# Kernel optimization log

Measured on AMD Instinct MI355X. Metric: run time of the kernel, lower is better.

Reference implementation:

```python
import jax, jax.numpy as jnp
import numpy as np

D_MODEL = 2048
N_Q_HEADS = 32
N_KV_HEADS = 8
HEAD_DIM = D_MODEL // N_Q_HEADS  # 64
KV_DIM = HEAD_DIM * N_KV_HEADS   # 512
B, S = 2, 2048


def setup_inputs() -> dict:
    key = jax.random.key(0)
    ks = jax.random.split(key, 11)
    sc_d = 1.0 / np.sqrt(D_MODEL)
    return {
        "query": jax.random.normal(ks[0], (B, S, D_MODEL), jnp.float32),
        "key":   jax.random.normal(ks[1], (B, S, D_MODEL), jnp.float32),
        "value": jax.random.normal(ks[2], (B, S, D_MODEL), jnp.float32),
        "Wq": jax.random.normal(ks[3], (D_MODEL, D_MODEL), jnp.float32) * sc_d,
        "bq": jnp.zeros((D_MODEL,), jnp.float32),
        "Wk": jax.random.normal(ks[4], (D_MODEL, KV_DIM), jnp.float32) * sc_d,
        "bk": jnp.zeros((KV_DIM,), jnp.float32),
        "Wv": jax.random.normal(ks[5], (D_MODEL, KV_DIM), jnp.float32) * sc_d,
        "bv": jnp.zeros((KV_DIM,), jnp.float32),
        "Wo": jax.random.normal(ks[6], (D_MODEL, D_MODEL), jnp.float32) * sc_d,
        "bo": jnp.zeros((D_MODEL,), jnp.float32),
    }


def reference(query, key, value, Wq, bq, Wk, bk, Wv, bv, Wo, bo):
    b, s, _ = query.shape
    g = N_Q_HEADS // N_KV_HEADS  # num groups
    # projections
    Q = query @ Wq + bq                      # [b, s, d_model]
    K = key @ Wk + bk                        # [b, s, kv_dim]
    V = value @ Wv + bv                      # [b, s, kv_dim]
    # split heads. Torch code splits Q into groups of num_kv_heads heads,
    # and each group broadcasts per-head against the Hkv KV heads, i.e.
    # query head (grp*Hkv + j) attends against kv head j.
    Q = Q.reshape(b, s, g, N_KV_HEADS, HEAD_DIM)  # [b, s, g, hkv, d]
    K = K.reshape(b, s, N_KV_HEADS, HEAD_DIM)     # [b, s, hkv, d]
    V = V.reshape(b, s, N_KV_HEADS, HEAD_DIM)
    scale = 1.0 / jnp.sqrt(jnp.float32(HEAD_DIM))
    scores = jnp.einsum('bsghd,bthd->bghst', Q, K) * scale  # [b,g,hkv,s,s]
    attn = jax.nn.softmax(scores, axis=-1)
    out = jnp.einsum('bghst,bthd->bsghd', attn, V)          # [b,s,g,hkv,d]
    # concat over groups then heads == original head order (g major, hkv minor)
    out = out.reshape(b, s, D_MODEL)
    return out @ Wo + bo
```

## Files before the change

kernel.cpp:

```cpp
#include <hip/hip_runtime.h>
#include <cstdint>

typedef _Float16 half4 __attribute__((ext_vector_type(4)));
typedef _Float16 half8 __attribute__((ext_vector_type(8)));
typedef _Float16 half16 __attribute__((ext_vector_type(16)));
typedef float f32x4 __attribute__((ext_vector_type(4)));
typedef float f32x16 __attribute__((ext_vector_type(16)));

#define L2E 1.44269504088896340736f

__device__ __forceinline__ void gl16(const void* g, void* l) {
  __builtin_amdgcn_global_load_lds(
      (const __attribute__((address_space(1))) void*)g,
      (__attribute__((address_space(3))) void*)l, 16, 0, 0);
}

__device__ __forceinline__ uint32_t pk2(float a, float b) {
  return __builtin_bit_cast(uint32_t, __builtin_amdgcn_cvt_pkrtz(a, b));
}

__device__ __forceinline__ void plswap(uint32_t& x, uint32_t& y) {
  auto r = __builtin_amdgcn_permlane32_swap((int)x, (int)y, false, false);
  x = (uint32_t)r[0];
  y = (uint32_t)r[1];
}

__device__ __forceinline__ f32x16 zero16() {
  f32x16 z;
  #pragma unroll
  for (int r = 0; r < 16; ++r) z[r] = 0.0f;
  return z;
}

__global__ __launch_bounds__(256) void cvt_f32_f16_3(
    const float* __restrict__ s0, const float* __restrict__ s1, const float* __restrict__ s2,
    _Float16* __restrict__ d0, _Float16* __restrict__ d1, _Float16* __restrict__ d2)
{
  const float* src = (blockIdx.z == 0) ? s0 : (blockIdx.z == 1 ? s1 : s2);
  _Float16* dst    = (blockIdx.z == 0) ? d0 : (blockIdx.z == 1 ? d1 : d2);
  size_t i = ((size_t)blockIdx.x * 256 + threadIdx.x) * 8;
  float4 a = *(const float4*)(src + i);
  float4 b = *(const float4*)(src + i + 4);
  half8 o;
  o[0] = (_Float16)a.x; o[1] = (_Float16)a.y; o[2] = (_Float16)a.z; o[3] = (_Float16)a.w;
  o[4] = (_Float16)b.x; o[5] = (_Float16)b.y; o[6] = (_Float16)b.z; o[7] = (_Float16)b.w;
  *(half8*)(dst + i) = o;
}

__global__ __launch_bounds__(256) void transpose_w_all(
    const float* __restrict__ Wq, const float* __restrict__ Wk,
    const float* __restrict__ Wv, const float* __restrict__ Wo,
    _Float16* __restrict__ WqkvT, _Float16* __restrict__ WoT)
{
  int id = blockIdx.x;
  const float* src;
  _Float16* dst;
  int N, tx, ty;
  if (id < 4096)      { src = Wq; dst = WqkvT;                        N = 2048; tx = id & 63; ty = id >> 6; }
  else if (id < 5120) { id -= 4096; src = Wk; dst = WqkvT + (size_t)2048 * 2048; N = 512; tx = id & 15; ty = id >> 4; }
  else if (id < 6144) { id -= 5120; src = Wv; dst = WqkvT + (size_t)2560 * 2048; N = 512; tx = id & 15; ty = id >> 4; }
  else                { id -= 6144; src = Wo; dst = WoT;              N = 2048; tx = id & 63; ty = id >> 6; }
  const int n0 = tx * 32, k0 = ty * 32;
  __shared__ float t[32][33];
  #pragma unroll
  for (int i = 0; i < 4; ++i)
    t[threadIdx.y + i * 8][threadIdx.x] =
        src[(size_t)(k0 + threadIdx.y + i * 8) * N + n0 + threadIdx.x];
  __syncthreads();
  #pragma unroll
  for (int i = 0; i < 4; ++i)
    dst[(size_t)(n0 + threadIdx.y + i * 8) * 2048 + k0 + threadIdx.x] =
        (_Float16)t[threadIdx.x][threadIdx.y + i * 8];
}

__global__ __launch_bounds__(256) void transpose_v(
    const _Float16* __restrict__ QKV, _Float16* __restrict__ VT)
{
  const int bh = blockIdx.z;
  const int bb = bh >> 3, h = bh & 7;
  const int t0 = blockIdx.x * 32, d0 = blockIdx.y * 32;
  __shared__ _Float16 t[32][33];
  const _Float16* src = QKV + (size_t)(bb * 2048) * 3072 + 2560 + h * 64;
  #pragma unroll
  for (int i = 0; i < 4; ++i)
    t[threadIdx.y + i * 8][threadIdx.x] =
        src[(size_t)(t0 + threadIdx.y + i * 8) * 3072 + d0 + threadIdx.x];
  __syncthreads();
  _Float16* dst = VT + ((size_t)(bb * 8 + h) * 64) * 2048;
  #pragma unroll
  for (int i = 0; i < 4; ++i)
    dst[(size_t)(d0 + threadIdx.y + i * 8) * 2048 + t0 + threadIdx.x] =
        t[threadIdx.x][threadIdx.y + i * 8];
}

template<int MODE>
__global__ __launch_bounds__(512, 2) void gemm256(
    const _Float16* __restrict__ Aq, const _Float16* __restrict__ Ak, const _Float16* __restrict__ Av,
    const _Float16* __restrict__ Bt,
    const float* __restrict__ bias0, const float* __restrict__ bias1, const float* __restrict__ bias2,
    _Float16* __restrict__ Ch, float* __restrict__ Cf)
{
  constexpr int K = 2048;
  constexpr int N = (MODE == 0) ? 3072 : 2048;
  constexpr int NB = N / 256;
  constexpr int G = 16 * NB;

  const int wg = blockIdx.x;
  const int work = (wg & 7) * (G / 8) + (wg >> 3);
  const int m0 = (work / NB) * 256;
  const int n0 = (work % NB) * 256;

  const _Float16* A = Aq;
  if constexpr (MODE == 0) { if (n0 >= 2560) A = Av; else if (n0 >= 2048) A = Ak; }

  const int tid = threadIdx.x;
  const int lane = tid & 63;
  const int w = tid >> 6;
  const int wr = w >> 2;
  const int wc = w & 3;
  const int lo = lane & 15, hi = lane >> 4;

  __shared__ __align__(1024) char smem[98304];

  f32x4 acc[8][4];
  #pragma unroll
  for (int mt = 0; mt < 8; ++mt)
    #pragma unroll
    for (int nt = 0; nt < 4; ++nt)
      acc[mt][nt] = (f32x4){0.f, 0.f, 0.f, 0.f};

  const int srow = lane >> 2;
  const int sslot = lane & 3;
  const _Float16* pA = A  + (size_t)(m0 + w * 32 + srow) * K + sslot * 8;
  const _Float16* pB = Bt + (size_t)(n0 + w * 32 + srow) * K + sslot * 8;
  const size_t rstep = (size_t)16 * K;
  const int dst = w * 2048;

  {
    char* b0 = smem;
    char* b1 = smem + 32768;
    gl16(pA,            b0 + dst);          gl16(pA + rstep,            b0 + dst + 1024);
    gl16(pB,            b0 + 16384 + dst);  gl16(pB + rstep,            b0 + 16384 + dst + 1024);
    gl16(pA + 32,       b1 + dst);          gl16(pA + 32 + rstep,       b1 + dst + 1024);
    gl16(pB + 32,       b1 + 16384 + dst);  gl16(pB + 32 + rstep,       b1 + 16384 + dst + 1024);
  }
  pA += 64; pB += 64;
  asm volatile("s_waitcnt vmcnt(4)" ::: "memory");
  __builtin_amdgcn_s_barrier();

  const int abase = (wr * 128 + lo) * 64 + hi * 16;
  const int bbase = 16384 + (wc * 64 + lo) * 64 + hi * 16;

  int c = 0;
  for (int t = 0; t < 64; ++t) {
    int c1 = c + 1; if (c1 == 3) c1 = 0;
    int c2 = c1 + 1; if (c2 == 3) c2 = 0;
    if (t < 62) {
      char* bp = smem + (c2 << 15);
      gl16(pA,         bp + dst);          gl16(pA + rstep,         bp + dst + 1024);
      gl16(pB,         bp + 16384 + dst);  gl16(pB + rstep,         bp + 16384 + dst + 1024);
      pA += 32; pB += 32;
    }
    const char* bc = smem + (c << 15);
    half8 af[8], bf[4];
    #pragma unroll
    for (int mt = 0; mt < 8; ++mt) af[mt] = *(const half8*)(bc + abase + mt * 1024);
    #pragma unroll
    for (int nt = 0; nt < 4; ++nt) bf[nt] = *(const half8*)(bc + bbase + nt * 1024);
    __builtin_amdgcn_s_setprio(1);
    #pragma unroll
    for (int mt = 0; mt < 8; ++mt)
      #pragma unroll
      for (int nt = 0; nt < 4; ++nt)
        acc[mt][nt] = __builtin_amdgcn_mfma_f32_16x16x32_f16(af[mt], bf[nt], acc[mt][nt], 0, 0, 0);
    __builtin_amdgcn_s_setprio(0);
    if (t < 62)       asm volatile("s_waitcnt vmcnt(4)" ::: "memory");
    else if (t == 62) asm volatile("s_waitcnt vmcnt(0)" ::: "memory");
    if (t < 63) __builtin_amdgcn_s_barrier();
    c = c1;
  }

  float* T = (float*)smem;
  const int tr = tid >> 4;
  const int sc = tid & 15;
  #pragma unroll
  for (int mp = 0; mp < 8; ++mp) {
    __syncthreads();
    #pragma unroll
    for (int nt = 0; nt < 4; ++nt)
      #pragma unroll
      for (int r = 0; r < 4; ++r)
        T[(wr * 16 + 4 * hi + r) * 256 + wc * 64 + nt * 16 + lo] = acc[mp][nt][r];
    __syncthreads();
    const int grow = m0 + (tr >> 4) * 128 + mp * 16 + (tr & 15);
    const int gcol = n0 + sc * 16;
    const float* Trow = T + tr * 256 + sc * 16;
    float4 v[4];
    #pragma unroll
    for (int q = 0; q < 4; ++q) v[q] = ((const float4*)Trow)[q];
    const float* bp = bias0;
    int cb = gcol;
    if constexpr (MODE == 0) {
      if (gcol >= 2560) { bp = bias2; cb = gcol - 2560; }
      else if (gcol >= 2048) { bp = bias1; cb = gcol - 2048; }
    }
    float4 bvv[4];
    #pragma unroll
    for (int q = 0; q < 4; ++q) bvv[q] = ((const float4*)(bp + cb))[q];
    if constexpr (MODE == 0) {
      half16 o;
      #pragma unroll
      for (int q = 0; q < 4; ++q) {
        o[4 * q + 0] = (_Float16)(v[q].x + bvv[q].x);
        o[4 * q + 1] = (_Float16)(v[q].y + bvv[q].y);
        o[4 * q + 2] = (_Float16)(v[q].z + bvv[q].z);
        o[4 * q + 3] = (_Float16)(v[q].w + bvv[q].w);
      }
      *(half16*)(Ch + (size_t)grow * N + gcol) = o;
    } else {
      float* dstp = Cf + (size_t)grow * N + gcol;
      #pragma unroll
      for (int q = 0; q < 4; ++q) {
        float4 ov = {v[q].x + bvv[q].x, v[q].y + bvv[q].y, v[q].z + bvv[q].z, v[q].w + bvv[q].w};
        ((float4*)dstp)[q] = ov;
      }
    }
  }
}

__global__ __launch_bounds__(256, 4) void attn_fwd4(
    const _Float16* __restrict__ QKV, const _Float16* __restrict__ VT,
    _Float16* __restrict__ AO)
{
  const int wg = blockIdx.x;
  const int work = (wg & 7) * 128 + (wg >> 3);
  const int bh = work >> 6;
  const int b = bh >> 3, h = bh & 7;
  const int rem = work & 63;
  const int qh = (rem >> 4) * 8 + h;
  const int qt = rem & 15;

  const int tid = threadIdx.x;
  const int lane = tid & 63;
  const int w = tid >> 6;
  const int l31 = lane & 31;
  const int hi5 = lane >> 5;
  const int r7 = l31 & 7;

  __shared__ __align__(1024) char sm[2][2][8192];

  const _Float16 QSC = (_Float16)(0.125f * L2E);
  const int qrow0 = b * 2048 + qt * 128 + w * 32 + l31;
  half8 qf[4];
  {
    const _Float16* qp = QKV + (size_t)qrow0 * 3072 + qh * 64 + hi5 * 8;
    #pragma unroll
    for (int s = 0; s < 4; ++s) {
      half8 q = *(const half8*)(qp + s * 16);
      #pragma unroll
      for (int e = 0; e < 8; ++e) q[e] = q[e] * QSC;
      qf[s] = q;
    }
  }

  const int li = lane >> 3;
  const int lc = lane & 7;
  const int kslot = lc ^ li;
  const int w16li = w * 16 + li;
  const _Float16* Ksrc = QKV + ((size_t)(b * 2048 + w16li)) * 3072 + 2048 + h * 64 + kslot * 8;
  const _Float16* Vsrc = VT + ((size_t)(b * 8 + h) * 64 + w16li) * 2048 + kslot * 8;

  f32x16 oa[2];
  oa[0] = zero16();
  oa[1] = zero16();
  float lreg = 0.f;

  {
    char* kd = &sm[0][0][0] + w * 2048;
    char* vd = &sm[0][1][0] + w * 2048;
    gl16(Ksrc, kd);
    gl16(Ksrc + (size_t)8 * 3072, kd + 1024);
    gl16(Vsrc, vd);
    gl16(Vsrc + (size_t)8 * 2048, vd + 1024);
  }
  __syncthreads();

  int cur = 0;
  for (int t = 0; t < 32; ++t) {
    if (t < 31) {
      const int t0 = (t + 1) * 64;
      char* kd = &sm[cur ^ 1][0][0] + w * 2048;
      char* vd = &sm[cur ^ 1][1][0] + w * 2048;
      const _Float16* kg = Ksrc + (size_t)t0 * 3072;
      const _Float16* vg = Vsrc + t0;
      gl16(kg, kd);
      gl16(kg + (size_t)8 * 3072, kd + 1024);
      gl16(vg, vd);
      gl16(vg + (size_t)8 * 2048, vd + 1024);
    }

    const char* Kb = &sm[cur][0][0];
    const char* Vb = &sm[cur][1][0];

    uint32_t pw[4][4];
    float ps = 0.f;
    #pragma unroll
    for (int j = 0; j < 2; ++j) {
      f32x16 sa = zero16();
      const int kr = j * 32 + l31;
      __builtin_amdgcn_s_setprio(1);
      #pragma unroll
      for (int s = 0; s < 4; ++s) {
        half8 kf = *(const half8*)(Kb + kr * 128 + (((2 * s + hi5) ^ r7) << 4));
        sa = __builtin_amdgcn_mfma_f32_32x32x16_f16(kf, qf[s], sa, 0, 0, 0);
      }
      __builtin_amdgcn_s_setprio(0);
      #pragma unroll
      for (int r = 0; r < 16; ++r) {
        const float p = __builtin_amdgcn_exp2f(sa[r]);
        sa[r] = p;
        ps += p;
      }
      #pragma unroll
      for (int hf = 0; hf < 2; ++hf) {
        const int rb = hf * 8;
        uint32_t w0 = pk2(sa[rb + 0], sa[rb + 1]);
        uint32_t w1 = pk2(sa[rb + 2], sa[rb + 3]);
        uint32_t w2 = pk2(sa[rb + 4], sa[rb + 5]);
        uint32_t w3 = pk2(sa[rb + 6], sa[rb + 7]);
        plswap(w0, w2);
        plswap(w1, w3);
        const int s = 2 * j + hf;
        pw[s][0] = w0; pw[s][1] = w1; pw[s][2] = w2; pw[s][3] = w3;
      }
    }
    ps += __shfl_xor(ps, 32);
    lreg += ps;

    __builtin_amdgcn_s_setprio(1);
    #pragma unroll
    for (int s = 0; s < 4; ++s) {
      union { uint32_t u[4]; half8 h; } p0;
      #pragma unroll
      for (int u = 0; u < 4; ++u) p0.u[u] = pw[s][u];
      #pragma unroll
      for (int i = 0; i < 2; ++i) {
        const int vr = i * 32 + l31;
        half8 vf = *(const half8*)(Vb + vr * 128 + (((2 * s + hi5) ^ r7) << 4));
        oa[i] = __builtin_amdgcn_mfma_f32_32x32x16_f16(vf, p0.h, oa[i], 0, 0, 0);
      }
    }
    __builtin_amdgcn_s_setprio(0);

    __syncthreads();
    cur ^= 1;
  }

  {
    const float inv = 1.0f / lreg;
    #pragma unroll
    for (int i = 0; i < 2; ++i) {
      _Float16* dst = AO + (size_t)qrow0 * 2048 + qh * 64 + i * 32 + hi5 * 4;
      #pragma unroll
      for (int q = 0; q < 4; ++q) {
        union { uint32_t u[2]; half4 h4; } o;
        o.u[0] = pk2(oa[i][4 * q + 0] * inv, oa[i][4 * q + 1] * inv);
        o.u[1] = pk2(oa[i][4 * q + 2] * inv, oa[i][4 * q + 3] * inv);
        *(half4*)(dst + 8 * q) = o.h4;
      }
    }
  }
}

extern "C" void kernel_launch(void* const* d_in, const int* in_sizes, int n_in,
                              void* d_out, int out_size, void* d_ws, size_t ws_size,
                              hipStream_t stream) {
  const float* query = (const float*)d_in[0];
  const float* key   = (const float*)d_in[1];
  const float* value = (const float*)d_in[2];
  const float* Wq = (const float*)d_in[3];
  const float* bq = (const float*)d_in[4];
  const float* Wk = (const float*)d_in[5];
  const float* bk = (const float*)d_in[6];
  const float* Wv = (const float*)d_in[7];
  const float* bv = (const float*)d_in[8];
  const float* Wo = (const float*)d_in[9];
  const float* bo = (const float*)d_in[10];
  float* out = (float*)d_out;

  char* ws = (char*)d_ws;
  _Float16* qh    = (_Float16*)(ws);
  _Float16* kh    = (_Float16*)(ws + 16777216);
  _Float16* vh    = (_Float16*)(ws + 33554432);
  _Float16* WqkvT = (_Float16*)(ws + 50331648);
  _Float16* WoT   = (_Float16*)(ws + 62914560);
  _Float16* QKVh  = (_Float16*)(ws + 71303168);
  _Float16* VT    = (_Float16*)(ws + 96468992);
  _Float16* aoh   = (_Float16*)(ws + 100663296);

  cvt_f32_f16_3<<<dim3(4096, 1, 3), 256, 0, stream>>>(query, key, value, qh, kh, vh);
  transpose_w_all<<<10240, dim3(32, 8), 0, stream>>>(Wq, Wk, Wv, Wo, WqkvT, WoT);
  gemm256<0><<<192, 512, 0, stream>>>(qh, kh, vh, WqkvT, bq, bk, bv, QKVh, nullptr);
  transpose_v<<<dim3(64, 2, 16), dim3(32, 8), 0, stream>>>(QKVh, VT);
  attn_fwd4<<<1024, 256, 0, stream>>>(QKVh, VT, aoh);
  gemm256<1><<<128, 512, 0, stream>>>(aoh, nullptr, nullptr, WoT, bo, nullptr, nullptr, nullptr, out);
}
```

Baseline: 260.9 us.

## Fuse fp32-to-fp16 activation conversion into QKV projection GEMM loads

Removes the separate conversion kernel and has the QKV GEMM stage fp32 activation tiles straight into LDS with a swizzled layout, converting to fp16 in registers before the MFMAs. This saves a full write and read-back of the fp16 activation copies, but doubles the A-tile LDS footprint, so the launch bound drops to one block per CU. The attention kernel's occupancy hint is also raised from 4 to 5 blocks.

After: 257.3 us. Within noise of the previous version (-1.4%).

```diff
diff --git a/kernel.cpp b/kernel.cpp
--- a/kernel.cpp
+++ b/kernel.cpp
@@ -30,21 +30,6 @@
   #pragma unroll
   for (int r = 0; r < 16; ++r) z[r] = 0.0f;
   return z;
-}
-
-__global__ __launch_bounds__(256) void cvt_f32_f16_3(
-    const float* __restrict__ s0, const float* __restrict__ s1, const float* __restrict__ s2,
-    _Float16* __restrict__ d0, _Float16* __restrict__ d1, _Float16* __restrict__ d2)
-{
-  const float* src = (blockIdx.z == 0) ? s0 : (blockIdx.z == 1 ? s1 : s2);
-  _Float16* dst    = (blockIdx.z == 0) ? d0 : (blockIdx.z == 1 ? d1 : d2);
-  size_t i = ((size_t)blockIdx.x * 256 + threadIdx.x) * 8;
-  float4 a = *(const float4*)(src + i);
-  float4 b = *(const float4*)(src + i + 4);
-  half8 o;
-  o[0] = (_Float16)a.x; o[1] = (_Float16)a.y; o[2] = (_Float16)a.z; o[3] = (_Float16)a.w;
-  o[4] = (_Float16)b.x; o[5] = (_Float16)b.y; o[6] = (_Float16)b.z; o[7] = (_Float16)b.w;
-  *(half8*)(dst + i) = o;
 }
 
 __global__ __launch_bounds__(256) void transpose_w_all(
@@ -94,8 +79,9 @@
 }
 
 template<int MODE>
-__global__ __launch_bounds__(512, 2) void gemm256(
-    const _Float16* __restrict__ Aq, const _Float16* __restrict__ Ak, const _Float16* __restrict__ Av,
+__global__ __launch_bounds__(512, 1) void gemm256(
+    const float* __restrict__ Fq, const float* __restrict__ Fk, const float* __restrict__ Fv,
+    const _Float16* __restrict__ Ah,
     const _Float16* __restrict__ Bt,
     const float* __restrict__ bias0, const float* __restrict__ bias1, const float* __restrict__ bias2,
     _Float16* __restrict__ Ch, float* __restrict__ Cf)
@@ -104,14 +90,17 @@
   constexpr int N = (MODE == 0) ? 3072 : 2048;
   constexpr int NB = N / 256;
   constexpr int G = 16 * NB;
+  constexpr int ABYTES = (MODE == 0) ? 32768 : 16384;
+  constexpr int BUF = ABYTES + 16384;
+  constexpr int NVM = (MODE == 0) ? 6 : 4;
 
   const int wg = blockIdx.x;
   const int work = (wg & 7) * (G / 8) + (wg >> 3);
   const int m0 = (work / NB) * 256;
   const int n0 = (work % NB) * 256;
 
-  const _Float16* A = Aq;
-  if constexpr (MODE == 0) { if (n0 >= 2560) A = Av; else if (n0 >= 2048) A = Ak; }
+  const float* Af = Fq;
+  if constexpr (MODE == 0) { if (n0 >= 2560) Af = Fv; else if (n0 >= 2048) Af = Fk; }
 
   const int tid = threadIdx.x;
   const int lane = tid & 63;
@@ -120,7 +109,7 @@
   const int wc = w & 3;
   const int lo = lane & 15, hi = lane >> 4;
 
-  __shared__ __align__(1024) char smem[98304];
+  __shared__ __align__(1024) char smem[3 * BUF];
 
   f32x4 acc[8][4];
   #pragma unroll
@@ -129,44 +118,84 @@
     for (int nt = 0; nt < 4; ++nt)
       acc[mt][nt] = (f32x4){0.f, 0.f, 0.f, 0.f};
 
-  const int srow = lane >> 2;
-  const int sslot = lane & 3;
-  const _Float16* pA = A  + (size_t)(m0 + w * 32 + srow) * K + sslot * 8;
-  const _Float16* pB = Bt + (size_t)(n0 + w * 32 + srow) * K + sslot * 8;
-  const size_t rstep = (size_t)16 * K;
-  const int dst = w * 2048;
-
-  {
-    char* b0 = smem;
-    char* b1 = smem + 32768;
-    gl16(pA,            b0 + dst);          gl16(pA + rstep,            b0 + dst + 1024);
-    gl16(pB,            b0 + 16384 + dst);  gl16(pB + rstep,            b0 + 16384 + dst + 1024);
-    gl16(pA + 32,       b1 + dst);          gl16(pA + 32 + rstep,       b1 + dst + 1024);
-    gl16(pB + 32,       b1 + 16384 + dst);  gl16(pB + 32 + rstep,       b1 + 16384 + dst + 1024);
-  }
-  pA += 64; pB += 64;
-  asm volatile("s_waitcnt vmcnt(4)" ::: "memory");
+  const _Float16* pB = Bt + (size_t)(n0 + w * 32 + (lane >> 2)) * K + (lane & 3) * 8;
+  const size_t bstep = (size_t)16 * K;
+  const int dstB = ABYTES + w * 2048;
+
+  const int li = lane >> 3;
+  const int kslot = (lane & 7) ^ li;
+  const float* pA32 = nullptr;
+  const _Float16* pA16 = nullptr;
+  if constexpr (MODE == 0)
+    pA32 = Af + (size_t)(m0 + w * 32 + li) * K + kslot * 4;
+  else
+    pA16 = Ah + (size_t)(m0 + w * 32 + (lane >> 2)) * K + (lane & 3) * 8;
+  const size_t a32step = (size_t)8 * K;
+  const int dstA = w * 4096;
+
+  #define STAGE_TILE(buf)                                                     \
+    do {                                                                      \
+      char* bp_ = smem + (buf) * BUF;                                         \
+      if constexpr (MODE == 0) {                                              \
+        gl16(pA32,               bp_ + dstA);                                 \
+        gl16(pA32 + a32step,     bp_ + dstA + 1024);                          \
+        gl16(pA32 + 2 * a32step, bp_ + dstA + 2048);                          \
+        gl16(pA32 + 3 * a32step, bp_ + dstA + 3072);                          \
+      } else {                                                                \
+        gl16(pA16,               bp_ + (w * 2048));                           \
+        gl16(pA16 + bstep,       bp_ + (w * 2048) + 1024);                    \
+      }                                                                       \
+      gl16(pB,         bp_ + dstB);                                           \
+      gl16(pB + bstep, bp_ + dstB + 1024);                                    \
+    } while (0)
+
+  #define ADVANCE()                                                           \
+    do {                                                                      \
+      if constexpr (MODE == 0) pA32 += 32; else pA16 += 32;                   \
+      pB += 32;                                                               \
+    } while (0)
+
+  STAGE_TILE(0); ADVANCE();
+  STAGE_TILE(1); ADVANCE();
+  asm volatile("s_waitcnt vmcnt(%0)" :: "i"(NVM) : "memory");
   __builtin_amdgcn_s_barrier();
 
-  const int abase = (wr * 128 + lo) * 64 + hi * 16;
-  const int bbase = 16384 + (wc * 64 + lo) * 64 + hi * 16;
+  const int sx = (lo & 7) << 4;
+  const int ao0 = ((2 * hi) << 4) ^ sx;
+  const int ao1 = ((2 * hi + 1) << 4) ^ sx;
+  const int arow0 = wr * 128 + lo;
+  const int abase16 = (wr * 128 + lo) * 64 + hi * 16;
+  const int bbase = ABYTES + (wc * 64 + lo) * 64 + hi * 16;
 
   int c = 0;
   for (int t = 0; t < 64; ++t) {
     int c1 = c + 1; if (c1 == 3) c1 = 0;
     int c2 = c1 + 1; if (c2 == 3) c2 = 0;
-    if (t < 62) {
-      char* bp = smem + (c2 << 15);
-      gl16(pA,         bp + dst);          gl16(pA + rstep,         bp + dst + 1024);
-      gl16(pB,         bp + 16384 + dst);  gl16(pB + rstep,         bp + 16384 + dst + 1024);
-      pA += 32; pB += 32;
-    }
-    const char* bc = smem + (c << 15);
+    if (t < 62) { STAGE_TILE(c2); ADVANCE(); }
+
+    const char* bc = smem + c * BUF;
     half8 af[8], bf[4];
-    #pragma unroll
-    for (int mt = 0; mt < 8; ++mt) af[mt] = *(const half8*)(bc + abase + mt * 1024);
+    if constexpr (MODE == 0) {
+      #pragma unroll
+      for (int mt = 0; mt < 8; ++mt) {
+        const char* rb = bc + (arow0 + mt * 16) * 128;
+        f32x4 a0 = *(const f32x4*)(rb + ao0);
+        f32x4 a1 = *(const f32x4*)(rb + ao1);
+        union { uint32_t u[4]; half8 h; } cv;
+        cv.u[0] = pk2(a0[0], a0[1]);
+        cv.u[1] = pk2(a0[2], a0[3]);
+        cv.u[2] = pk2(a1[0], a1[1]);
+        cv.u[3] = pk2(a1[2], a1[3]);
+        af[mt] = cv.h;
+      }
+    } else {
+      #pragma unroll
+      for (int mt = 0; mt < 8; ++mt)
+        af[mt] = *(const half8*)(bc + abase16 + mt * 1024);
+    }
     #pragma unroll
     for (int nt = 0; nt < 4; ++nt) bf[nt] = *(const half8*)(bc + bbase + nt * 1024);
+
     __builtin_amdgcn_s_setprio(1);
     #pragma unroll
     for (int mt = 0; mt < 8; ++mt)
@@ -174,11 +203,14 @@
       for (int nt = 0; nt < 4; ++nt)
         acc[mt][nt] = __builtin_amdgcn_mfma_f32_16x16x32_f16(af[mt], bf[nt], acc[mt][nt], 0, 0, 0);
     __builtin_amdgcn_s_setprio(0);
-    if (t < 62)       asm volatile("s_waitcnt vmcnt(4)" ::: "memory");
+
+    if (t < 62)       asm volatile("s_waitcnt vmcnt(%0)" :: "i"(NVM) : "memory");
     else if (t == 62) asm volatile("s_waitcnt vmcnt(0)" ::: "memory");
     if (t < 63) __builtin_amdgcn_s_barrier();
     c = c1;
   }
+  #undef STAGE_TILE
+  #undef ADVANCE
 
   float* T = (float*)smem;
   const int tr = tid >> 4;
@@ -228,7 +260,7 @@
   }
 }
 
-__global__ __launch_bounds__(256, 4) void attn_fwd4(
+__global__ __launch_bounds__(256, 5) void attn_fwd4(
     const _Float16* __restrict__ QKV, const _Float16* __restrict__ VT,
     _Float16* __restrict__ AO)
 {
@@ -389,19 +421,17 @@
   float* out = (float*)d_out;
 
   char* ws = (char*)d_ws;
-  _Float16* qh    = (_Float16*)(ws);
-  _Float16* kh    = (_Float16*)(ws + 16777216);
-  _Float16* vh    = (_Float16*)(ws + 33554432);
   _Float16* WqkvT = (_Float16*)(ws + 50331648);
   _Float16* WoT   = (_Float16*)(ws + 62914560);
   _Float16* QKVh  = (_Float16*)(ws + 71303168);
   _Float16* VT    = (_Float16*)(ws + 96468992);
   _Float16* aoh   = (_Float16*)(ws + 100663296);
 
-  cvt_f32_f16_3<<<dim3(4096, 1, 3), 256, 0, stream>>>(query, key, value, qh, kh, vh);
   transpose_w_all<<<10240, dim3(32, 8), 0, stream>>>(Wq, Wk, Wv, Wo, WqkvT, WoT);
-  gemm256<0><<<192, 512, 0, stream>>>(qh, kh, vh, WqkvT, bq, bk, bv, QKVh, nullptr);
+  gemm256<0><<<192, 512, 0, stream>>>(query, key, value, nullptr, WqkvT,
+                                      bq, bk, bv, QKVh, nullptr);
   transpose_v<<<dim3(64, 2, 16), dim3(32, 8), 0, stream>>>(QKVh, VT);
   attn_fwd4<<<1024, 256, 0, stream>>>(QKVh, VT, aoh);
-  gemm256<1><<<128, 512, 0, stream>>>(aoh, nullptr, nullptr, WoT, bo, nullptr, nullptr, nullptr, out);
-}
+  gemm256<1><<<128, 512, 0, stream>>>(nullptr, nullptr, nullptr, aoh, WoT,
+                                      bo, nullptr, nullptr, nullptr, out);
+}
```

## Shrink GEMM M-tile to 128 rows to double block count

Applied to the files above, without the earlier changes.

Both projection GEMMs now use 128x256 tiles instead of 256x256, doubling the grid (384 and 256 blocks) so more of the 256 CUs get work. Shared memory per stage and the accumulator register file shrink, and the load and epilogue loops are adjusted to match. The attention kernel's launch bounds are also raised to 5 blocks per SM, which may force tighter register allocation. Smaller tiles lower arithmetic intensity per byte loaded from global memory.

Result: faster. 248.2 us (-4.9%).

```diff
diff --git a/kernel.cpp b/kernel.cpp
--- a/kernel.cpp
+++ b/kernel.cpp
@@ -94,7 +94,7 @@
 }
 
 template<int MODE>
-__global__ __launch_bounds__(512, 2) void gemm256(
+__global__ __launch_bounds__(512, 2) void gemm128(
     const _Float16* __restrict__ Aq, const _Float16* __restrict__ Ak, const _Float16* __restrict__ Av,
     const _Float16* __restrict__ Bt,
     const float* __restrict__ bias0, const float* __restrict__ bias1, const float* __restrict__ bias2,
@@ -103,11 +103,12 @@
   constexpr int K = 2048;
   constexpr int N = (MODE == 0) ? 3072 : 2048;
   constexpr int NB = N / 256;
-  constexpr int G = 16 * NB;
+  constexpr int G = 32 * NB;
+  constexpr int BUF = 8192 + 16384;
 
   const int wg = blockIdx.x;
   const int work = (wg & 7) * (G / 8) + (wg >> 3);
-  const int m0 = (work / NB) * 256;
+  const int m0 = (work / NB) * 128;
   const int n0 = (work % NB) * 256;
 
   const _Float16* A = Aq;
@@ -120,61 +121,60 @@
   const int wc = w & 3;
   const int lo = lane & 15, hi = lane >> 4;
 
-  __shared__ __align__(1024) char smem[98304];
-
-  f32x4 acc[8][4];
-  #pragma unroll
-  for (int mt = 0; mt < 8; ++mt)
+  __shared__ __align__(1024) char smem[3 * BUF];
+
+  f32x4 acc[4][4];
+  #pragma unroll
+  for (int mt = 0; mt < 4; ++mt)
     #pragma unroll
     for (int nt = 0; nt < 4; ++nt)
       acc[mt][nt] = (f32x4){0.f, 0.f, 0.f, 0.f};
 
-  const int srow = lane >> 2;
-  const int sslot = lane & 3;
-  const _Float16* pA = A  + (size_t)(m0 + w * 32 + srow) * K + sslot * 8;
-  const _Float16* pB = Bt + (size_t)(n0 + w * 32 + srow) * K + sslot * 8;
-  const size_t rstep = (size_t)16 * K;
-  const int dst = w * 2048;
-
-  {
-    char* b0 = smem;
-    char* b1 = smem + 32768;
-    gl16(pA,            b0 + dst);          gl16(pA + rstep,            b0 + dst + 1024);
-    gl16(pB,            b0 + 16384 + dst);  gl16(pB + rstep,            b0 + 16384 + dst + 1024);
-    gl16(pA + 32,       b1 + dst);          gl16(pA + 32 + rstep,       b1 + dst + 1024);
-    gl16(pB + 32,       b1 + 16384 + dst);  gl16(pB + 32 + rstep,       b1 + 16384 + dst + 1024);
-  }
+  const _Float16* pB = Bt + (size_t)(n0 + w * 32 + (lane >> 2)) * K + (lane & 3) * 8;
+  const _Float16* pA = A  + (size_t)(m0 + w * 16 + (lane >> 2)) * K + (lane & 3) * 8;
+  const size_t bstep = (size_t)16 * K;
+  const int dstB = 8192 + w * 2048;
+  const int dstA = w * 1024;
+
+  gl16(pA,      smem + dstA);
+  gl16(pB,      smem + dstB);        gl16(pB + bstep,      smem + dstB + 1024);
+  gl16(pA + 32, smem + BUF + dstA);
+  gl16(pB + 32, smem + BUF + dstB);  gl16(pB + 32 + bstep, smem + BUF + dstB + 1024);
   pA += 64; pB += 64;
-  asm volatile("s_waitcnt vmcnt(4)" ::: "memory");
+  asm volatile("s_waitcnt vmcnt(3)" ::: "memory");
   __builtin_amdgcn_s_barrier();
 
-  const int abase = (wr * 128 + lo) * 64 + hi * 16;
-  const int bbase = 16384 + (wc * 64 + lo) * 64 + hi * 16;
+  const int abase = (wr * 64 + lo) * 64 + hi * 16;
+  const int bbase = 8192 + (wc * 64 + lo) * 64 + hi * 16;
 
   int c = 0;
   for (int t = 0; t < 64; ++t) {
     int c1 = c + 1; if (c1 == 3) c1 = 0;
     int c2 = c1 + 1; if (c2 == 3) c2 = 0;
     if (t < 62) {
-      char* bp = smem + (c2 << 15);
-      gl16(pA,         bp + dst);          gl16(pA + rstep,         bp + dst + 1024);
-      gl16(pB,         bp + 16384 + dst);  gl16(pB + rstep,         bp + 16384 + dst + 1024);
+      char* bp_ = smem + c2 * BUF;
+      gl16(pA, bp_ + dstA);
+      gl16(pB, bp_ + dstB);
+      gl16(pB + bstep, bp_ + dstB + 1024);
       pA += 32; pB += 32;
     }
-    const char* bc = smem + (c << 15);
-    half8 af[8], bf[4];
-    #pragma unroll
-    for (int mt = 0; mt < 8; ++mt) af[mt] = *(const half8*)(bc + abase + mt * 1024);
+
+    const char* bc = smem + c * BUF;
+    half8 af[4], bf[4];
+    #pragma unroll
+    for (int mt = 0; mt < 4; ++mt) af[mt] = *(const half8*)(bc + abase + mt * 1024);
     #pragma unroll
     for (int nt = 0; nt < 4; ++nt) bf[nt] = *(const half8*)(bc + bbase + nt * 1024);
+
     __builtin_amdgcn_s_setprio(1);
     #pragma unroll
-    for (int mt = 0; mt < 8; ++mt)
+    for (int mt = 0; mt < 4; ++mt)
       #pragma unroll
       for (int nt = 0; nt < 4; ++nt)
         acc[mt][nt] = __builtin_amdgcn_mfma_f32_16x16x32_f16(af[mt], bf[nt], acc[mt][nt], 0, 0, 0);
     __builtin_amdgcn_s_setprio(0);
-    if (t < 62)       asm volatile("s_waitcnt vmcnt(4)" ::: "memory");
+
+    if (t < 62)       asm volatile("s_waitcnt vmcnt(3)" ::: "memory");
     else if (t == 62) asm volatile("s_waitcnt vmcnt(0)" ::: "memory");
     if (t < 63) __builtin_amdgcn_s_barrier();
     c = c1;
@@ -184,7 +184,7 @@
   const int tr = tid >> 4;
   const int sc = tid & 15;
   #pragma unroll
-  for (int mp = 0; mp < 8; ++mp) {
+  for (int mp = 0; mp < 4; ++mp) {
     __syncthreads();
     #pragma unroll
     for (int nt = 0; nt < 4; ++nt)
@@ -192,7 +192,7 @@
       for (int r = 0; r < 4; ++r)
         T[(wr * 16 + 4 * hi + r) * 256 + wc * 64 + nt * 16 + lo] = acc[mp][nt][r];
     __syncthreads();
-    const int grow = m0 + (tr >> 4) * 128 + mp * 16 + (tr & 15);
+    const int grow = m0 + (tr >> 4) * 64 + mp * 16 + (tr & 15);
     const int gcol = n0 + sc * 16;
     const float* Trow = T + tr * 256 + sc * 16;
     float4 v[4];
@@ -228,7 +228,7 @@
   }
 }
 
-__global__ __launch_bounds__(256, 4) void attn_fwd4(
+__global__ __launch_bounds__(256, 5) void attn_fwd4(
     const _Float16* __restrict__ QKV, const _Float16* __restrict__ VT,
     _Float16* __restrict__ AO)
 {
@@ -400,8 +400,9 @@
 
   cvt_f32_f16_3<<<dim3(4096, 1, 3), 256, 0, stream>>>(query, key, value, qh, kh, vh);
   transpose_w_all<<<10240, dim3(32, 8), 0, stream>>>(Wq, Wk, Wv, Wo, WqkvT, WoT);
-  gemm256<0><<<192, 512, 0, stream>>>(qh, kh, vh, WqkvT, bq, bk, bv, QKVh, nullptr);
+  gemm128<0><<<384, 512, 0, stream>>>(qh, kh, vh, WqkvT, bq, bk, bv, QKVh, nullptr);
   transpose_v<<<dim3(64, 2, 16), dim3(32, 8), 0, stream>>>(QKVh, VT);
   attn_fwd4<<<1024, 256, 0, stream>>>(QKVh, VT, aoh);
-  gemm256<1><<<128, 512, 0, stream>>>(aoh, nullptr, nullptr, WoT, bo, nullptr, nullptr, nullptr, out);
-}
+  gemm128<1><<<256, 512, 0, stream>>>(aoh, nullptr, nullptr, WoT, bo,
+                                      nullptr, nullptr, nullptr, out);
+}
```
